# Optimization experiments

Hardware: AMD Instinct MI355X
Metric: run time of the kernel (lower is better)

## Reference

```python
import jax, jax.numpy as jnp
import numpy as np

N_NODES = 100000
EMB_DIM = 128
HIDDEN = 64
N_EDGES = 1600000


def setup_inputs() -> dict:
    key = jax.random.key(0)
    k_emb, k_ei, k_w1, k_b1, k_w2, k_b2 = jax.random.split(key, 6)
    node_embeddings = jax.random.normal(k_emb, (N_NODES, EMB_DIM), dtype=jnp.float32)
    edge_index = jax.random.randint(k_ei, (2, N_EDGES), 0, N_NODES, dtype=jnp.int64)
    in_dim = 2 * EMB_DIM
    # Kaiming-uniform-ish init like torch Linear
    lim1 = 1.0 / np.sqrt(in_dim)
    lim2 = 1.0 / np.sqrt(HIDDEN)
    W1 = jax.random.uniform(k_w1, (in_dim, HIDDEN), minval=-lim1, maxval=lim1, dtype=jnp.float32)
    b1 = jax.random.uniform(k_b1, (HIDDEN,), minval=-lim1, maxval=lim1, dtype=jnp.float32)
    W2 = jax.random.uniform(k_w2, (HIDDEN, 1), minval=-lim2, maxval=lim2, dtype=jnp.float32)
    b2 = jax.random.uniform(k_b2, (1,), minval=-lim2, maxval=lim2, dtype=jnp.float32)
    return {"node_embeddings": node_embeddings, "edge_index": edge_index,
            "W1": W1, "b1": b1, "W2": W2, "b2": b2}


def reference(node_embeddings, edge_index, W1, b1, W2, b2):
    # Gather source/target node embeddings per edge
    src = node_embeddings[edge_index[0]]            # [E, D]
    tgt = node_embeddings[edge_index[1]]            # [E, D]
    edge_features = jnp.concatenate([src, tgt], axis=1)  # [E, 2D]
    h = jax.nn.relu(edge_features @ W1 + b1)        # [E, H]; dropout = identity (eval)
    edge_scores = (h @ W2 + b2).squeeze(-1)         # [E]
    return edge_scores
```

## Files before the change

### kernel.cpp

```cpp
#include <hip/hip_runtime.h>
#include <hip/hip_bf16.h>

typedef float f32x4 __attribute__((ext_vector_type(4)));
typedef __bf16 bf16x8 __attribute__((ext_vector_type(8)));
typedef _Float16 f16x2 __attribute__((ext_vector_type(2)));
typedef _Float16 f16x8 __attribute__((ext_vector_type(8)));
typedef unsigned short u16;

__device__ inline u16 f2bf(float f) {
    unsigned int u = __float_as_uint(f);
    return (u16)((u + 0x7fffu + ((u >> 16) & 1u)) >> 16);
}

__device__ inline bf16x8 pack8(const float4 a, const float4 b) {
    union { u16 h[8]; bf16x8 v; } r;
    r.h[0] = f2bf(a.x); r.h[1] = f2bf(a.y); r.h[2] = f2bf(a.z); r.h[3] = f2bf(a.w);
    r.h[4] = f2bf(b.x); r.h[5] = f2bf(b.y); r.h[6] = f2bf(b.z); r.h[7] = f2bf(b.w);
    return r.v;
}

__global__ __launch_bounds__(256) void cvt_w_kernel(const float* __restrict__ W1,
                                                    u16* __restrict__ wf) {
    int i = blockIdx.x * 256 + threadIdx.x;
    if (i >= 128 * 128) return;
    int j = i & 7, fl = i >> 3;
    int lane = fl & 63, kbt = fl >> 6;
    int kb = kbt >> 3, t = kbt & 7;
    int k = kb * 32 + ((lane >> 4) & 3) * 8 + j;
    int n = t * 16 + (lane & 15);
    int krow = k + ((n >= 64) ? 128 : 0);
    wf[i] = f2bf(W1[krow * 64 + (n & 63)]);
}

__global__ __launch_bounds__(256) void uv_gemm_kernel(
    const float* __restrict__ emb, const u16* __restrict__ wf,
    _Float16* __restrict__ uv, int M) {
    __shared__ __align__(16) u16 bsh[32 * 64 * 8];

    const int tid = threadIdx.x;
    const int w = tid >> 6, lane = tid & 63, quad = lane >> 4, l15 = lane & 15;
    {
        const uint4* s = (const uint4*)wf;
        uint4* d = (uint4*)bsh;
#pragma unroll
        for (int i = 0; i < 8; ++i) d[tid + i * 256] = s[tid + i * 256];
    }
    __syncthreads();

    const int rb = blockIdx.x * 128 + w * 32;

    bf16x8 a[2][4];
#pragma unroll
    for (int m = 0; m < 2; ++m) {
        int row = rb + m * 16 + l15;
        if (row >= M) row = M - 1;
        const float* p = emb + (long)row * 128 + quad * 8;
#pragma unroll
        for (int kb = 0; kb < 4; ++kb) {
            float4 x = ((const float4*)(p + kb * 32))[0];
            float4 y = ((const float4*)(p + kb * 32))[1];
            a[m][kb] = pack8(x, y);
        }
    }

    f32x4 acc[2][8];
#pragma unroll
    for (int m = 0; m < 2; ++m)
#pragma unroll
        for (int t = 0; t < 8; ++t)
#pragma unroll
            for (int r = 0; r < 4; ++r) acc[m][t][r] = 0.0f;

#pragma unroll
    for (int kb = 0; kb < 4; ++kb)
#pragma unroll
        for (int t = 0; t < 8; ++t) {
            bf16x8 bf = *(const bf16x8*)(bsh + ((kb * 8 + t) * 64 + lane) * 8);
#pragma unroll
            for (int m = 0; m < 2; ++m)
                acc[m][t] = __builtin_amdgcn_mfma_f32_16x16x32_bf16(a[m][kb], bf,
                                                                    acc[m][t], 0, 0, 0);
        }

#pragma unroll
    for (int m = 0; m < 2; ++m)
#pragma unroll
        for (int t = 0; t < 8; ++t)
#pragma unroll
            for (int r = 0; r < 4; ++r) {
                int row = rb + m * 16 + quad * 4 + r;
                if (row < M) uv[(long)row * 128 + t * 16 + l15] = (_Float16)acc[m][t][r];
            }
}

__device__ inline f16x2 relu2(f16x2 x) {
    f16x2 r;
    r[0] = (x[0] > (_Float16)0.f) ? x[0] : (_Float16)0.f;
    r[1] = (x[1] > (_Float16)0.f) ? x[1] : (_Float16)0.f;
    return r;
}

__global__ __launch_bounds__(256, 8) void edge_score_kernel(
    const _Float16* __restrict__ uv, const int* __restrict__ idx,
    const float* __restrict__ b1, const float* __restrict__ w2,
    const float* __restrict__ b2, float* __restrict__ out, int E, int nT) {
    const int tid = threadIdx.x, w = tid >> 6, lane = tid & 63;
    const int e4 = lane >> 2, q = lane & 3;

    f16x2 b1h[8], w2h[8];
#pragma unroll
    for (int i = 0; i < 4; ++i) {
        b1h[i][0]     = (_Float16)b1[q * 8 + 2 * i];
        b1h[i][1]     = (_Float16)b1[q * 8 + 2 * i + 1];
        b1h[4 + i][0] = (_Float16)b1[32 + q * 8 + 2 * i];
        b1h[4 + i][1] = (_Float16)b1[32 + q * 8 + 2 * i + 1];
        w2h[i][0]     = (_Float16)w2[q * 8 + 2 * i];
        w2h[i][1]     = (_Float16)w2[q * 8 + 2 * i + 1];
        w2h[4 + i][0] = (_Float16)w2[32 + q * 8 + 2 * i];
        w2h[4 + i][1] = (_Float16)w2[32 + q * 8 + 2 * i + 1];
    }
    const float b2v = b2[0];

    const int gw = blockIdx.x * 4 + w, stride = gridDim.x * 4;
    const int step = stride * 2;

    auto ldidx = [&](int tile, int& s, int& t) {
        int e = tile * 16 + e4;
        if (e >= E) e = E - 1;
        s = __builtin_nontemporal_load(idx + e);
        t = __builtin_nontemporal_load(idx + E + e);
    };

    union F8 { f16x8 v; f16x2 p[4]; };

    auto score16 = [&](int src, int tgt) -> float {
        const _Float16* up = uv + (long)src * 128;
        const _Float16* vp = uv + (long)tgt * 128;
        F8 U0, U1, V0, V1;
        U0.v = *(const f16x8*)(up + q * 8);
        U1.v = *(const f16x8*)(up + 32 + q * 8);
        V0.v = *(const f16x8*)(vp + 64 + q * 8);
        V1.v = *(const f16x8*)(vp + 96 + q * 8);
        float s = 0.f;
#pragma unroll
        for (int i = 0; i < 4; ++i) {
            f16x2 h = relu2((U0.p[i] + V0.p[i]) + b1h[i]);
#if __has_builtin(__builtin_amdgcn_fdot2)
            s = __builtin_amdgcn_fdot2(h, w2h[i], s, false);
#else
            s += (float)h[0] * (float)w2h[i][0] + (float)h[1] * (float)w2h[i][1];
#endif
        }
#pragma unroll
        for (int i = 0; i < 4; ++i) {
            f16x2 h = relu2((U1.p[i] + V1.p[i]) + b1h[4 + i]);
#if __has_builtin(__builtin_amdgcn_fdot2)
            s = __builtin_amdgcn_fdot2(h, w2h[4 + i], s, false);
#else
            s += (float)h[0] * (float)w2h[4 + i][0] + (float)h[1] * (float)w2h[4 + i][1];
#endif
        }
        return s;
    };

    int sA, tA, sB, tB;
    {
        int t0 = (gw < nT) ? gw : 0;
        int t1 = (gw + stride < nT) ? (gw + stride) : t0;
        ldidx(t0, sA, tA);
        ldidx(t1, sB, tB);
    }

    for (int tile = gw; tile < nT; tile += step) {
        const int tileB = tile + stride;

        int n0 = tile + step, n1 = tile + step + stride;
        int sA2, tA2, sB2, tB2;
        ldidx(n0 < nT ? n0 : tile, sA2, tA2);
        ldidx(n1 < nT ? n1 : tile, sB2, tB2);

        float sa = score16(sA, tA);
        float sb = score16(sB, tB);

        sa += __shfl_xor(sa, 1, 64);
        sa += __shfl_xor(sa, 2, 64);
        sb += __shfl_xor(sb, 1, 64);
        sb += __shfl_xor(sb, 2, 64);

        if (q == 0) {
            int ea = tile * 16 + e4;
            if (ea < E) __builtin_nontemporal_store(sa + b2v, out + ea);
            if (tileB < nT) {
                int eb = tileB * 16 + e4;
                if (eb < E) __builtin_nontemporal_store(sb + b2v, out + eb);
            }
        }
        sA = sA2; tA = tA2; sB = sB2; tB = tB2;
    }
}

extern "C" void kernel_launch(void* const* d_in, const int* in_sizes, int n_in,
                              void* d_out, int out_size, void* d_ws, size_t ws_size,
                              hipStream_t stream) {
    const float* emb_f = (const float*)d_in[0];
    const int*   idx   = (const int*)d_in[1];
    const float* W1    = (const float*)d_in[2];
    const float* b1    = (const float*)d_in[3];
    const float* W2    = (const float*)d_in[4];
    const float* b2    = (const float*)d_in[5];
    float* out = (float*)d_out;

    const int embN = in_sizes[0];
    const int M    = embN / 128;
    const int E    = in_sizes[1] / 2;

    _Float16* uv = (_Float16*)d_ws;
    u16* wf = (u16*)(uv + (long)M * 128);

    cvt_w_kernel<<<64, 256, 0, stream>>>(W1, wf);
    uv_gemm_kernel<<<(M + 127) / 128, 256, 0, stream>>>(emb_f, wf, uv, M);

    int nT = (E + 15) / 16;
    edge_score_kernel<<<2048, 256, 0, stream>>>(uv, idx, b1, W2, b2, out, E, nT);
}
```

Measured before the change: 160.0 us.

## Fold b1 into node GEMM, vectorize UV stores, use hardware pack conversions

```diff
diff --git a/kernel.cpp b/kernel.cpp
--- a/kernel.cpp
+++ b/kernel.cpp
@@ -4,6 +4,7 @@
 typedef float f32x4 __attribute__((ext_vector_type(4)));
 typedef __bf16 bf16x8 __attribute__((ext_vector_type(8)));
 typedef _Float16 f16x2 __attribute__((ext_vector_type(2)));
+typedef _Float16 f16x4 __attribute__((ext_vector_type(4)));
 typedef _Float16 f16x8 __attribute__((ext_vector_type(8)));
 typedef unsigned short u16;
 
@@ -12,11 +13,10 @@
     return (u16)((u + 0x7fffu + ((u >> 16) & 1u)) >> 16);
 }
 
-__device__ inline bf16x8 pack8(const float4 a, const float4 b) {
-    union { u16 h[8]; bf16x8 v; } r;
-    r.h[0] = f2bf(a.x); r.h[1] = f2bf(a.y); r.h[2] = f2bf(a.z); r.h[3] = f2bf(a.w);
-    r.h[4] = f2bf(b.x); r.h[5] = f2bf(b.y); r.h[6] = f2bf(b.z); r.h[7] = f2bf(b.w);
-    return r.v;
+__device__ inline f16x2 pkrtz(float a, float b) {
+    union { __fp16 h __attribute__((ext_vector_type(2))); f16x2 f; } r;
+    r.h = __builtin_amdgcn_cvt_pkrtz(a, b);
+    return r.f;
 }
 
 __global__ __launch_bounds__(256) void cvt_w_kernel(const float* __restrict__ W1,
@@ -32,9 +32,18 @@
     wf[i] = f2bf(W1[krow * 64 + (n & 63)]);
 }
 
+__device__ inline bf16x8 pack8(const float4 a, const float4 b) {
+    union { unsigned int w[4]; bf16x8 v; } r;
+    asm("v_cvt_pk_bf16_f32 %0, %1, %2" : "=v"(r.w[0]) : "v"(a.x), "v"(a.y));
+    asm("v_cvt_pk_bf16_f32 %0, %1, %2" : "=v"(r.w[1]) : "v"(a.z), "v"(a.w));
+    asm("v_cvt_pk_bf16_f32 %0, %1, %2" : "=v"(r.w[2]) : "v"(b.x), "v"(b.y));
+    asm("v_cvt_pk_bf16_f32 %0, %1, %2" : "=v"(r.w[3]) : "v"(b.z), "v"(b.w));
+    return r.v;
+}
+
 __global__ __launch_bounds__(256) void uv_gemm_kernel(
     const float* __restrict__ emb, const u16* __restrict__ wf,
-    _Float16* __restrict__ uv, int M) {
+    const float* __restrict__ b1, _Float16* __restrict__ uv, int M) {
     __shared__ __align__(16) u16 bsh[32 * 64 * 8];
 
     const int tid = threadIdx.x;
@@ -82,15 +91,27 @@
                                                                     acc[m][t], 0, 0, 0);
         }
 
+    float b1c[4];
+#pragma unroll
+    for (int t = 0; t < 4; ++t) b1c[t] = b1[t * 16 + l15];
+
 #pragma unroll
     for (int m = 0; m < 2; ++m)
 #pragma unroll
-        for (int t = 0; t < 8; ++t)
-#pragma unroll
-            for (int r = 0; r < 4; ++r) {
-                int row = rb + m * 16 + quad * 4 + r;
-                if (row < M) uv[(long)row * 128 + t * 16 + l15] = (_Float16)acc[m][t][r];
-            }
+        for (int r = 0; r < 4; ++r) {
+            int node = rb + m * 16 + quad * 4 + r;
+            if (node >= M) continue;
+            f16x2 u0 = pkrtz(acc[m][0][r] + b1c[0], acc[m][1][r] + b1c[1]);
+            f16x2 u1 = pkrtz(acc[m][2][r] + b1c[2], acc[m][3][r] + b1c[3]);
+            f16x2 v0 = pkrtz(acc[m][4][r], acc[m][5][r]);
+            f16x2 v1 = pkrtz(acc[m][6][r], acc[m][7][r]);
+            f16x4 su, sv;
+            su[0] = u0[0]; su[1] = u0[1]; su[2] = u1[0]; su[3] = u1[1];
+            sv[0] = v0[0]; sv[1] = v0[1]; sv[2] = v1[0]; sv[3] = v1[1];
+            _Float16* p = uv + (long)node * 128 + l15 * 4;
+            *(f16x4*)p = su;
+            *(f16x4*)(p + 64) = sv;
+        }
 }
 
 __device__ inline f16x2 relu2(f16x2 x) {
@@ -100,24 +121,29 @@
     return r;
 }
 
+__device__ inline float dot2(f16x2 h, f16x2 w, float s) {
+#if __has_builtin(__builtin_amdgcn_fdot2)
+    return __builtin_amdgcn_fdot2(h, w, s, false);
+#else
+    return s + (float)h[0] * (float)w[0] + (float)h[1] * (float)w[1];
+#endif
+}
+
 __global__ __launch_bounds__(256, 8) void edge_score_kernel(
     const _Float16* __restrict__ uv, const int* __restrict__ idx,
-    const float* __restrict__ b1, const float* __restrict__ w2,
-    const float* __restrict__ b2, float* __restrict__ out, int E, int nT) {
+    const float* __restrict__ w2, const float* __restrict__ b2,
+    float* __restrict__ out, int E, int nT) {
     const int tid = threadIdx.x, w = tid >> 6, lane = tid & 63;
     const int e4 = lane >> 2, q = lane & 3;
 
-    f16x2 b1h[8], w2h[8];
-#pragma unroll
-    for (int i = 0; i < 4; ++i) {
-        b1h[i][0]     = (_Float16)b1[q * 8 + 2 * i];
-        b1h[i][1]     = (_Float16)b1[q * 8 + 2 * i + 1];
-        b1h[4 + i][0] = (_Float16)b1[32 + q * 8 + 2 * i];
-        b1h[4 + i][1] = (_Float16)b1[32 + q * 8 + 2 * i + 1];
-        w2h[i][0]     = (_Float16)w2[q * 8 + 2 * i];
-        w2h[i][1]     = (_Float16)w2[q * 8 + 2 * i + 1];
-        w2h[4 + i][0] = (_Float16)w2[32 + q * 8 + 2 * i];
-        w2h[4 + i][1] = (_Float16)w2[32 + q * 8 + 2 * i + 1];
+    f16x2 w2h[8];
+#pragma unroll
+    for (int i = 0; i < 8; ++i) {
+        int s0 = 2 * i, s1 = 2 * i + 1;
+        int d0 = ((s0 & 3) << 4) + (q << 2) + (s0 >> 2);
+        int d1 = ((s1 & 3) << 4) + (q << 2) + (s1 >> 2);
+        w2h[i][0] = (_Float16)w2[d0];
+        w2h[i][1] = (_Float16)w2[d1];
     }
     const float b2v = b2[0];
 
@@ -134,31 +160,23 @@
     union F8 { f16x8 v; f16x2 p[4]; };
 
     auto score16 = [&](int src, int tgt) -> float {
-        const _Float16* up = uv + (long)src * 128;
-        const _Float16* vp = uv + (long)tgt * 128;
+        const _Float16* up = uv + (long)src * 128 + q * 16;
+        const _Float16* vp = uv + (long)tgt * 128 + 64 + q * 16;
         F8 U0, U1, V0, V1;
-        U0.v = *(const f16x8*)(up + q * 8);
-        U1.v = *(const f16x8*)(up + 32 + q * 8);
-        V0.v = *(const f16x8*)(vp + 64 + q * 8);
-        V1.v = *(const f16x8*)(vp + 96 + q * 8);
+        U0.v = *(const f16x8*)up;
+        U1.v = *(const f16x8*)(up + 8);
+        V0.v = *(const f16x8*)vp;
+        V1.v = *(const f16x8*)(vp + 8);
         float s = 0.f;
 #pragma unroll
         for (int i = 0; i < 4; ++i) {
-            f16x2 h = relu2((U0.p[i] + V0.p[i]) + b1h[i]);
-#if __has_builtin(__builtin_amdgcn_fdot2)
-            s = __builtin_amdgcn_fdot2(h, w2h[i], s, false);
-#else
-            s += (float)h[0] * (float)w2h[i][0] + (float)h[1] * (float)w2h[i][1];
-#endif
+            f16x2 h = relu2(U0.p[i] + V0.p[i]);
+            s = dot2(h, w2h[i], s);
         }
 #pragma unroll
         for (int i = 0; i < 4; ++i) {
-            f16x2 h = relu2((U1.p[i] + V1.p[i]) + b1h[4 + i]);
-#if __has_builtin(__builtin_amdgcn_fdot2)
-            s = __builtin_amdgcn_fdot2(h, w2h[4 + i], s, false);
-#else
-            s += (float)h[0] * (float)w2h[4 + i][0] + (float)h[1] * (float)w2h[4 + i][1];
-#endif
+            f16x2 h = relu2(U1.p[i] + V1.p[i]);
+            s = dot2(h, w2h[4 + i], s);
         }
         return s;
     };
@@ -218,8 +236,8 @@
     u16* wf = (u16*)(uv + (long)M * 128);
 
     cvt_w_kernel<<<64, 256, 0, stream>>>(W1, wf);
-    uv_gemm_kernel<<<(M + 127) / 128, 256, 0, stream>>>(emb_f, wf, uv, M);
+    uv_gemm_kernel<<<(M + 127) / 128, 256, 0, stream>>>(emb_f, wf, b1, uv, M);
 
     int nT = (E + 15) / 16;
-    edge_score_kernel<<<2048, 256, 0, stream>>>(uv, idx, b1, W2, b2, out, E, nT);
-}
+    edge_score_kernel<<<2048, 256, 0, stream>>>(uv, idx, W2, b2, out, E, nT);
+}
```

Result: no change. 158.7 us (-0.8%).
